# Performance work log

Measured on AMD Instinct MI355X. Metric: run time of the kernel, lower is better.

Reference implementation:

```python
import jax, jax.numpy as jnp
import numpy as np
from functools import partial


def deform_sample(inp, dy, dx):
    """Bilinear sample inp[b,c] at (y+dy[b,c,y,x], x+dx[b,c,y,x]) with zero padding.
    inp, dy, dx: [B, C, H, W] -> [B, C, H, W]. Matches torchvision deform_conv2d
    with 1x1 kernel and offset_groups == C (one offset pair per channel)."""
    B, C, H, W = inp.shape
    ys = jnp.arange(H, dtype=inp.dtype)[None, None, :, None] + dy  # [B,C,H,W]
    xs = jnp.arange(W, dtype=inp.dtype)[None, None, None, :] + dx
    y0f = jnp.floor(ys)
    x0f = jnp.floor(xs)
    wy = ys - y0f
    wx = xs - x0f
    y0 = y0f.astype(jnp.int32)
    x0 = x0f.astype(jnp.int32)
    flat = inp.reshape(B, C, H * W)

    def gather(yi, xi):
        valid = (yi >= 0) & (yi < H) & (xi >= 0) & (xi < W)
        idx = jnp.clip(yi, 0, H - 1) * W + jnp.clip(xi, 0, W - 1)
        v = jnp.take_along_axis(flat, idx.reshape(B, C, H * W), axis=2).reshape(B, C, H, W)
        return jnp.where(valid, v, jnp.zeros((), inp.dtype))

    return ((1 - wy) * (1 - wx) * gather(y0, x0)
            + (1 - wy) * wx * gather(y0, x0 + 1)
            + wy * (1 - wx) * gather(y0 + 1, x0)
            + wy * wx * gather(y0 + 1, x0 + 1))


def atm_layer(x, offset, w_weight, w_bias, h_weight, h_bias, local_weight, local_bias,
              fc1_w, fc1_b, fc2_w, fc2_b, proj_w, proj_b):
    B, H, W, C = x.shape
    x_nchw = jnp.transpose(x, (0, 3, 1, 2))  # [B,C,H,W]
    zeros = jnp.zeros_like(x_nchw)

    # ATM along w: offset[:, :C] is x-offset (offset_t[:,1::2]), y-offset 0
    sw = deform_sample(x_nchw, zeros, offset[:, :C])
    w = jnp.einsum('bchw,oc->bhwo', sw, w_weight) + w_bias  # [B,H,W,C]

    # ATM along h: offset[:, C:] is y-offset (offset_t[:,0::2]), x-offset 0
    sh = deform_sample(x_nchw, offset[:, C:], zeros)
    h = jnp.einsum('bchw,oc->bhwo', sh, h_weight) + h_bias

    # depthwise 5x5 conv, padding 2
    c = jax.lax.conv_general_dilated(
        x_nchw, local_weight, window_strides=(1, 1), padding=((2, 2), (2, 2)),
        feature_group_count=C, dimension_numbers=('NCHW', 'OIHW', 'NCHW'))
    c = jnp.transpose(c, (0, 2, 3, 1)) + local_bias  # [B,H,W,C]

    # gating MLP: global average -> fc1 -> GELU -> fc2 -> softmax over 3 branches
    a = (w + h + c).mean(axis=(1, 2))  # [B,C]
    a = jax.nn.gelu(a @ fc1_w.T + fc1_b, approximate=False)
    a = a @ fc2_w.T + fc2_b  # [B,3C]
    a = jnp.transpose(a.reshape(B, C, 3), (2, 0, 1))  # [3,B,C]
    a = jax.nn.softmax(a, axis=0)[:, :, None, None, :]  # [3,B,1,1,C]

    out = w * a[0] + h * a[1] + c * a[2]
    out = out @ proj_w.T + proj_b
    return out


def setup_inputs() -> dict:
    C = 256
    B, H, W = 16, 64, 64
    key = jax.random.key(0)
    ks = jax.random.split(key, 16)
    bnd = 1.0 / np.sqrt(C)
    hid = C // 4
    return {
        'x': jax.random.normal(ks[0], (B, H, W, C), jnp.float32),
        'offset': jax.random.normal(ks[1], (B, 2 * C, H, W), jnp.float32),
        'w_weight': jax.random.uniform(ks[2], (C, C), jnp.float32, -bnd, bnd),
        'w_bias': jax.random.uniform(ks[3], (C,), jnp.float32, -bnd, bnd),
        'h_weight': jax.random.uniform(ks[4], (C, C), jnp.float32, -bnd, bnd),
        'h_bias': jax.random.uniform(ks[5], (C,), jnp.float32, -bnd, bnd),
        'local_weight': jax.random.uniform(ks[6], (C, 1, 5, 5), jnp.float32, -0.2, 0.2),
        'local_bias': jax.random.uniform(ks[7], (C,), jnp.float32, -0.2, 0.2),
        'fc1_w': jax.random.uniform(ks[8], (hid, C), jnp.float32, -bnd, bnd),
        'fc1_b': jax.random.uniform(ks[9], (hid,), jnp.float32, -bnd, bnd),
        'fc2_w': jax.random.uniform(ks[10], (3 * C, hid), jnp.float32, -1.0 / np.sqrt(hid), 1.0 / np.sqrt(hid)),
        'fc2_b': jax.random.uniform(ks[11], (3 * C,), jnp.float32, -1.0 / np.sqrt(hid), 1.0 / np.sqrt(hid)),
        'proj_w': jax.random.uniform(ks[12], (C, C), jnp.float32, -bnd, bnd),
        'proj_b': jax.random.uniform(ks[13], (C,), jnp.float32, -bnd, bnd),
    }


def reference(x, offset, w_weight, w_bias, h_weight, h_bias, local_weight, local_bias,
              fc1_w, fc1_b, fc2_w, fc2_b, proj_w, proj_b):
    return atm_layer(x, offset, w_weight, w_bias, h_weight, h_bias, local_weight,
                     local_bias, fc1_w, fc1_b, fc2_w, fc2_b, proj_w, proj_b)
```

## Files before the change

### kernel.cpp

```cpp
#include <hip/hip_runtime.h>
#include <hip/hip_bf16.h>

typedef _Float16 half4_t __attribute__((ext_vector_type(4)));
typedef _Float16 half8 __attribute__((ext_vector_type(8)));
typedef float f32x4 __attribute__((ext_vector_type(4)));

#define BB 16
#define HH 64
#define WW2 64
#define CC 256

__global__ __launch_bounds__(256) void k_pre(
    const float* __restrict__ Ww, const float* __restrict__ Wh,
    const float* __restrict__ pw,
    _Float16* __restrict__ WwT, _Float16* __restrict__ WhT,
    _Float16* __restrict__ pf, float* __restrict__ sums)
{
  __shared__ _Float16 tile[64][65];
  const int blk = blockIdx.x;
  const int t = threadIdx.x;

  if (blk < 32) {
    const int nt = blk & 3, kt = (blk >> 2) & 3, mat = blk >> 4;
    const float* src = mat ? Wh : Ww;
    _Float16* dst = mat ? WhT : WwT;
    const int n0 = nt * 64, k0 = kt * 64;
    const int sl = t & 63;
    #pragma unroll
    for (int p = 0; p < 16; p++) {
      int chl = (t >> 6) + p * 4;
      tile[chl][sl] = (_Float16)src[(size_t)(n0 + chl) * 256 + k0 + sl];
    }
    __syncthreads();
    #pragma unroll
    for (int p = 0; p < 2; p++) {
      int pl = (t >> 3) + p * 32;
      int c8 = (t & 7) * 8;
      half8 hv;
      #pragma unroll
      for (int r = 0; r < 8; r++) hv[r] = tile[c8 + r][pl];
      *(half8*)(dst + (size_t)(k0 + pl) * 256 + n0 + c8) = hv;
    }
  } else if (blk < 80) {
    sums[(blk - 32) * 256 + t] = 0.f;
  } else {
    int i = (blk - 80) * 2048 + t * 8;
    float4 v0 = *(const float4*)(pw + i);
    float4 v1 = *(const float4*)(pw + i + 4);
    half8 h = {(_Float16)v0.x, (_Float16)v0.y, (_Float16)v0.z, (_Float16)v0.w,
               (_Float16)v1.x, (_Float16)v1.y, (_Float16)v1.z, (_Float16)v1.w};
    *(half8*)(pf + i) = h;
  }
}

__global__ __launch_bounds__(256) void k_trans(const float* __restrict__ off,
                                               _Float16* __restrict__ offAT,
                                               _Float16* __restrict__ offBT)
{
  __shared__ _Float16 tile[64][65];
  const int blk = blockIdx.x;
  const int st   = blk & 63;
  const int cht  = (blk >> 6) & 3;
  const int half = (blk >> 8) & 1;
  const int b    = blk >> 9;
  const int t = threadIdx.x;

  const int s0 = st * 64;
  const int ch0 = half * 256 + cht * 64;
  const float* src = off + ((size_t)b * 512 + ch0) * 4096 + s0;
  const int sl = t & 63;
  #pragma unroll
  for (int p = 0; p < 16; p++) {
    int chl = (t >> 6) + p * 4;
    tile[chl][sl] = (_Float16)src[(size_t)chl * 4096 + sl];
  }
  __syncthreads();

  _Float16* dst = (half == 0) ? offAT : offBT;
  #pragma unroll
  for (int p = 0; p < 2; p++) {
    int pl = (t >> 3) + p * 32;
    int c8 = (t & 7) * 8;
    half8 hv;
    #pragma unroll
    for (int r = 0; r < 8; r++) hv[r] = tile[c8 + r][pl];
    int s = s0 + pl;
    size_t pix = (half == 0) ? ((size_t)b * 4096 + s)
                             : ((size_t)b * 4096 + (s & 63) * 64 + (s >> 6));
    *(half8*)(dst + pix * 256 + cht * 64 + c8) = hv;
  }
}

__global__ __launch_bounds__(256) void k_samp(
    const float* __restrict__ x, const _Float16* __restrict__ offA,
    const float* __restrict__ lw,
    _Float16* __restrict__ swb, _Float16* __restrict__ cvb,
    float* __restrict__ ssw, float* __restrict__ scv)
{
  __shared__ _Float16 xr[WW2 * CC];

  const int work = (blockIdx.x & 7) * 128 + (blockIdx.x >> 3);
  const int b = work >> 6, y = work & 63;
  const int t = threadIdx.x;
  const int c = t;

  const float* xrow_src = x + (size_t)(b * HH + y) * WW2 * CC;
  #pragma unroll
  for (int p = 0; p < 16; p++) {
    int i = p * 1024 + t * 4;
    float4 v = *(const float4*)(xrow_src + i);
    half4_t h = {(_Float16)v.x, (_Float16)v.y, (_Float16)v.z, (_Float16)v.w};
    *(half4_t*)(xr + i) = h;
  }

  float wgt[25];
  #pragma unroll
  for (int q = 0; q < 25; q++) wgt[q] = lw[c * 25 + q];

  const float* xb = x + (size_t)b * HH * WW2 * CC + c;
  const float* rp[5];
  bool yv[5];
  #pragma unroll
  for (int ky = 0; ky < 5; ky++) {
    int yy = y + ky - 2;
    yv[ky] = (yy >= 0 && yy < HH);
    rp[ky] = xb + (size_t)(yv[ky] ? yy : 0) * WW2 * CC;
  }

  _Float16* cp = cvb + ((size_t)b * 4096 + y * 64) * CC + c;
  float acc5[5] = {0.f, 0.f, 0.f, 0.f, 0.f};
  float acv = 0.f;

  #pragma unroll 5
  for (int u = 0; u < 70; ++u) {
    acc5[(u + 2) % 5] = 0.f;
    if (u < 64) {
      float c0 = yv[0] ? rp[0][u * CC] : 0.f;
      float c1 = yv[1] ? rp[1][u * CC] : 0.f;
      float c2 = yv[2] ? rp[2][u * CC] : 0.f;
      float c3 = yv[3] ? rp[3][u * CC] : 0.f;
      float c4 = yv[4] ? rp[4][u * CC] : 0.f;
      #pragma unroll
      for (int kx = 0; kx < 5; kx++) {
        acc5[(u + 7 - kx) % 5] += wgt[0 + kx] * c0 + wgt[5 + kx] * c1 +
                                  wgt[10 + kx] * c2 + wgt[15 + kx] * c3 +
                                  wgt[20 + kx] * c4;
      }
    }
    int xi = u - 2;
    if (xi >= 0 && xi < 64) {
      float cv = acc5[(u + 3) % 5];
      cp[(size_t)xi * CC] = (_Float16)cv;
      acv += cv;
    }
  }
  atomicAdd(&scv[b * CC + c], acv);

  __syncthreads();

  const _Float16* op = offA + ((size_t)b * 4096 + y * 64) * CC + c;
  _Float16* sp = swb + ((size_t)b * 4096 + y * 64) * CC + c;
  float asw = 0.f;

  #pragma unroll 8
  for (int xi = 0; xi < 64; xi++) {
    float dx = (float)op[(size_t)xi * CC];
    float xs = (float)xi + dx;
    float xf = floorf(xs);
    float wx = xs - xf;
    int xq = (int)xf;
    float v0 = (xq >= 0 && xq < WW2) ? (float)xr[xq * CC + c] : 0.f;
    float v1 = (xq + 1 >= 0 && xq + 1 < WW2) ? (float)xr[(xq + 1) * CC + c] : 0.f;
    float swv = (1.f - wx) * v0 + wx * v1;
    sp[(size_t)xi * CC] = (_Float16)swv;
    asw += swv;
  }
  atomicAdd(&ssw[b * CC + c], asw);
}

__global__ __launch_bounds__(256) void k_col(
    const float* __restrict__ x, const _Float16* __restrict__ offBT,
    _Float16* __restrict__ shb, float* __restrict__ ssh)
{
  __shared__ _Float16 xc[HH * CC];
  const int work = (blockIdx.x & 7) * 128 + (blockIdx.x >> 3);
  const int b = work >> 6, xi = work & 63;
  const int t = threadIdx.x;
  const int c = t;

  #pragma unroll
  for (int p = 0; p < 16; p++) {
    int yy = p * 4 + (t >> 6);
    int c4 = (t & 63) * 4;
    float4 v = *(const float4*)(x + ((size_t)(b * HH + yy) * WW2 + xi) * CC + c4);
    half4_t h = {(_Float16)v.x, (_Float16)v.y, (_Float16)v.z, (_Float16)v.w};
    *(half4_t*)(xc + yy * CC + c4) = h;
  }
  __syncthreads();

  const _Float16* obt = offBT + ((size_t)(b * WW2 + xi) * HH) * CC + c;
  _Float16* hp = shb + ((size_t)(b * HH) * WW2 + xi) * CC + c;
  float ash = 0.f;
  #pragma unroll 8
  for (int yy = 0; yy < 64; yy++) {
    float dy = (float)obt[(size_t)yy * CC];
    float ys = (float)yy + dy;
    float yf = floorf(ys);
    float wy = ys - yf;
    int yq = (int)yf;
    float u0 = (yq >= 0 && yq < HH) ? (float)xc[yq * CC + c] : 0.f;
    float u1 = (yq + 1 >= 0 && yq + 1 < HH) ? (float)xc[(yq + 1) * CC + c] : 0.f;
    float shv = (1.f - wy) * u0 + wy * u1;
    hp[(size_t)yy * WW2 * CC] = (_Float16)shv;
    ash += shv;
  }
  atomicAdd(&ssh[b * CC + c], ash);
}

__global__ __launch_bounds__(256) void k_gate(
    const float* __restrict__ ssw, const float* __restrict__ ssh, const float* __restrict__ scv,
    const float* __restrict__ Ww, const float* __restrict__ bw,
    const float* __restrict__ Wh, const float* __restrict__ bh,
    const float* __restrict__ blc,
    const float* __restrict__ fc1w, const float* __restrict__ fc1b,
    const float* __restrict__ fc2w, const float* __restrict__ fc2b,
    _Float16* __restrict__ gh, float* __restrict__ bcomb)
{
  __shared__ float sswl[CC], sshl[CC], avgl[CC], tl[64];
  const int b = blockIdx.x, tid = threadIdx.x;
  sswl[tid] = ssw[b * CC + tid];
  sshl[tid] = ssh[b * CC + tid];
  __syncthreads();

  float acc = scv[b * CC + tid];
  for (int c = 0; c < CC; c++)
    acc += sswl[c] * Ww[tid * CC + c] + sshl[c] * Wh[tid * CC + c];
  avgl[tid] = acc * (1.f / (HH * WW2)) + bw[tid] + bh[tid] + blc[tid];
  __syncthreads();

  if (tid < 64) {
    float a = fc1b[tid];
    for (int o = 0; o < CC; o++) a += avgl[o] * fc1w[tid * CC + o];
    tl[tid] = 0.5f * a * (1.f + erff(a * 0.70710678118654752f));
  }
  __syncthreads();

  float g[3];
  #pragma unroll
  for (int j = 0; j < 3; j++) {
    float a = fc2b[tid * 3 + j];
    for (int k = 0; k < 64; k++) a += tl[k] * fc2w[(tid * 3 + j) * 64 + k];
    g[j] = a;
  }
  float m = fmaxf(g[0], fmaxf(g[1], g[2]));
  float e0 = expf(g[0] - m), e1 = expf(g[1] - m), e2 = expf(g[2] - m);
  float inv = 1.f / (e0 + e1 + e2);
  float a0 = e0 * inv, a1 = e1 * inv, a2 = e2 * inv;
  gh[(0 * BB + b) * CC + tid] = (_Float16)a0;
  gh[(1 * BB + b) * CC + tid] = (_Float16)a1;
  gh[(2 * BB + b) * CC + tid] = (_Float16)a2;
  bcomb[b * CC + tid] = a0 * bw[tid] + a1 * bh[tid] + a2 * blc[tid];
}

__global__ __launch_bounds__(256) void k_mats(
    const _Float16* __restrict__ pf, const _Float16* __restrict__ gh,
    const _Float16* __restrict__ WwT, const _Float16* __restrict__ WhT,
    const float* __restrict__ bcomb, const float* __restrict__ pb,
    _Float16* __restrict__ Bcat, float* __restrict__ bias_out)
{
  const int blk = (blockIdx.x & 7) * 16 + (blockIdx.x >> 3);
  const int ob = blk & 3;
  const int br = (blk >> 2) & 1;
  const int b  = blk >> 3;
  const int o0 = ob * 64;
  const int tid = threadIdx.x;
  const int wid = tid >> 6, l = tid & 63;
  const int n0 = wid * 64;
  const int lr = l & 15;
  const int kg = (l >> 4) * 8;
  const int jr = (l >> 4) * 4;

  const _Float16* WT  = br ? WhT : WwT;
  const _Float16* ghb = gh + (size_t)(br * BB + b) * CC;

  f32x4 acc[4][4];
  #pragma unroll
  for (int mi = 0; mi < 4; mi++)
    #pragma unroll
    for (int ni = 0; ni < 4; ni++) acc[mi][ni] = (f32x4){0.f, 0.f, 0.f, 0.f};

  #pragma unroll
  for (int ks = 0; ks < 8; ks++) {
    half8 gv = *(const half8*)(ghb + kg + ks * 32);
    half8 a[4], bbv[4];
    #pragma unroll
    for (int mi = 0; mi < 4; mi++)
      a[mi] = *(const half8*)(pf + (size_t)(o0 + mi * 16 + lr) * CC + kg + ks * 32) * gv;
    #pragma unroll
    for (int ni = 0; ni < 4; ni++)
      bbv[ni] = *(const half8*)(WT + (size_t)(n0 + ni * 16 + lr) * CC + kg + ks * 32);
    #pragma unroll
    for (int mi = 0; mi < 4; mi++)
      #pragma unroll
      for (int ni = 0; ni < 4; ni++)
        acc[mi][ni] = __builtin_amdgcn_mfma_f32_16x16x32_f16(a[mi], bbv[ni], acc[mi][ni], 0, 0, 0);
  }

  #pragma unroll
  for (int ni = 0; ni < 4; ni++) {
    int kcol = n0 + ni * 16 + lr;
    #pragma unroll
    for (int mi = 0; mi < 4; mi++) {
      #pragma unroll
      for (int j = 0; j < 4; j++) {
        int o = o0 + mi * 16 + jr + j;
        Bcat[((size_t)b * CC + o) * 512 + br * 256 + kcol] = (_Float16)acc[mi][ni][j];
      }
    }
  }

  if (br == 0) {
    int o_l = tid >> 2, part = tid & 3;
    const _Float16* pr = pf + (size_t)(o0 + o_l) * CC + part * 64;
    const float* bc = bcomb + b * CC + part * 64;
    float s = 0.f;
    #pragma unroll
    for (int i = 0; i < 8; i++) {
      half8 h = *(const half8*)(pr + i * 8);
      #pragma unroll
      for (int r = 0; r < 8; r++) s += (float)h[r] * bc[i * 8 + r];
    }
    s += __shfl_xor(s, 1);
    s += __shfl_xor(s, 2);
    if (part == 0) bias_out[b * CC + o0 + o_l] = s + pb[o0 + o_l];
  }
}

#define APAD 264
__global__ __launch_bounds__(256) void k_gemm(
    const _Float16* __restrict__ swb, const _Float16* __restrict__ shb,
    const _Float16* __restrict__ cvb, const _Float16* __restrict__ Bcat,
    const _Float16* __restrict__ pf, const _Float16* __restrict__ a2h,
    const float* __restrict__ bias_out, float* __restrict__ out)
{
  __shared__ _Float16 smem[64 * APAD];

  const int work = (blockIdx.x & 7) * 128 + (blockIdx.x >> 3);
  const int r0 = work * 64;
  const int b = work >> 6;
  const int tid = threadIdx.x;
  const int wid = tid >> 6, l = tid & 63;
  const int n0 = wid * 64;
  const int lr = l & 15;
  const int kg = (l >> 4) * 8;
  const int jr = (l >> 4) * 4;

  const _Float16* bq = Bcat + ((size_t)b * CC + n0 + lr) * 512 + kg;

  f32x4 acc[4][4];
  #pragma unroll
  for (int mi = 0; mi < 4; mi++)
    #pragma unroll
    for (int ni = 0; ni < 4; ni++) acc[mi][ni] = (f32x4){0.f, 0.f, 0.f, 0.f};

  half8 st[8];
  {
    const _Float16* g = swb + (size_t)r0 * CC;
    #pragma unroll
    for (int p = 0; p < 8; p++) st[p] = *(const half8*)(g + p * 2048 + tid * 8);
    #pragma unroll
    for (int p = 0; p < 8; p++) {
      int i = p * 2048 + tid * 8;
      *(half8*)(smem + (i >> 8) * APAD + (i & 255)) = st[p];
    }
  }
  __syncthreads();
  {
    const _Float16* g = shb + (size_t)r0 * CC;
    #pragma unroll
    for (int p = 0; p < 8; p++) st[p] = *(const half8*)(g + p * 2048 + tid * 8);
  }
  #pragma unroll
  for (int ks = 0; ks < 8; ks++) {
    half8 a[4], bbv[4];
    #pragma unroll
    for (int mi = 0; mi < 4; mi++)
      a[mi] = *(const half8*)(smem + (mi * 16 + lr) * APAD + kg + ks * 32);
    #pragma unroll
    for (int ni = 0; ni < 4; ni++)
      bbv[ni] = *(const half8*)(bq + (size_t)ni * 16 * 512 + ks * 32);
    #pragma unroll
    for (int mi = 0; mi < 4; mi++)
      #pragma unroll
      for (int ni = 0; ni < 4; ni++)
        acc[mi][ni] = __builtin_amdgcn_mfma_f32_16x16x32_f16(a[mi], bbv[ni], acc[mi][ni], 0, 0, 0);
  }
  __syncthreads();
  #pragma unroll
  for (int p = 0; p < 8; p++) {
    int i = p * 2048 + tid * 8;
    *(half8*)(smem + (i >> 8) * APAD + (i & 255)) = st[p];
  }
  __syncthreads();
  {
    const _Float16* g = cvb + (size_t)r0 * CC;
    #pragma unroll
    for (int p = 0; p < 8; p++) st[p] = *(const half8*)(g + p * 2048 + tid * 8);
  }
  #pragma unroll
  for (int ks = 0; ks < 8; ks++) {
    half8 a[4], bbv[4];
    #pragma unroll
    for (int mi = 0; mi < 4; mi++)
      a[mi] = *(const half8*)(smem + (mi * 16 + lr) * APAD + kg + ks * 32);
    #pragma unroll
    for (int ni = 0; ni < 4; ni++)
      bbv[ni] = *(const half8*)(bq + (size_t)ni * 16 * 512 + 256 + ks * 32);
    #pragma unroll
    for (int mi = 0; mi < 4; mi++)
      #pragma unroll
      for (int ni = 0; ni < 4; ni++)
        acc[mi][ni] = __builtin_amdgcn_mfma_f32_16x16x32_f16(a[mi], bbv[ni], acc[mi][ni], 0, 0, 0);
  }
  __syncthreads();
  #pragma unroll
  for (int p = 0; p < 8; p++) {
    int i = p * 2048 + tid * 8;
    *(half8*)(smem + (i >> 8) * APAD + (i & 255)) = st[p];
  }
  __syncthreads();
  const _Float16* a2b = a2h + (size_t)b * CC;
  #pragma unroll
  for (int ks = 0; ks < 8; ks++) {
    half8 a2v = *(const half8*)(a2b + kg + ks * 32);
    half8 a[4], bbv[4];
    #pragma unroll
    for (int mi = 0; mi < 4; mi++)
      a[mi] = *(const half8*)(smem + (mi * 16 + lr) * APAD + kg + ks * 32);
    #pragma unroll
    for (int ni = 0; ni < 4; ni++)
      bbv[ni] = *(const half8*)(pf + (size_t)(n0 + ni * 16 + lr) * CC + kg + ks * 32) * a2v;
    #pragma unroll
    for (int mi = 0; mi < 4; mi++)
      #pragma unroll
      for (int ni = 0; ni < 4; ni++)
        acc[mi][ni] = __builtin_amdgcn_mfma_f32_16x16x32_f16(a[mi], bbv[ni], acc[mi][ni], 0, 0, 0);
  }

  #pragma unroll
  for (int ni = 0; ni < 4; ni++) {
    int col = n0 + ni * 16 + lr;
    float bo = bias_out[b * CC + col];
    #pragma unroll
    for (int mi = 0; mi < 4; mi++) {
      #pragma unroll
      for (int j = 0; j < 4; j++) {
        size_t idx = (size_t)(r0 + mi * 16 + jr + j) * CC + col;
        out[idx] = acc[mi][ni][j] + bo;
      }
    }
  }
}

extern "C" void kernel_launch(void* const* d_in, const int* in_sizes, int n_in,
                              void* d_out, int out_size, void* d_ws, size_t ws_size,
                              hipStream_t stream)
{
  const float* x    = (const float*)d_in[0];
  const float* off  = (const float*)d_in[1];
  const float* Ww   = (const float*)d_in[2];
  const float* bw   = (const float*)d_in[3];
  const float* Wh   = (const float*)d_in[4];
  const float* bh   = (const float*)d_in[5];
  const float* lw   = (const float*)d_in[6];
  const float* blc  = (const float*)d_in[7];
  const float* fc1w = (const float*)d_in[8];
  const float* fc1b = (const float*)d_in[9];
  const float* fc2w = (const float*)d_in[10];
  const float* fc2b = (const float*)d_in[11];
  const float* pw   = (const float*)d_in[12];
  const float* pb   = (const float*)d_in[13];
  float* out = (float*)d_out;

  char* ws = (char*)d_ws;
  _Float16* shb   = (_Float16*)(ws + 0);
  _Float16* offAT = (_Float16*)(ws + 33554432);
  _Float16* offBT = (_Float16*)(ws + 67108864);
  _Float16* swb   = (_Float16*)(ws + 67108864);
  _Float16* Bcat  = (_Float16*)(ws + 100663296);
  _Float16* cvb   = (_Float16*)(ws + 104857600);
  _Float16* pf    = (_Float16*)(ws + 138412032);
  _Float16* gh    = (_Float16*)(ws + 138543104);
  float* bcomb    = (float*)(ws + 138567680);
  float* bias_out = (float*)(ws + 138584064);
  _Float16* WwT = (_Float16*)((char*)d_out + 0);
  _Float16* WhT = (_Float16*)((char*)d_out + 131072);
  float* sums   = (float*)((char*)d_out + 262144);
  float* ssw = sums, *ssh = sums + 4096, *scv = sums + 8192;

  k_pre<<<112, 256, 0, stream>>>(Ww, Wh, pw, WwT, WhT, pf, sums);
  k_trans<<<8192, 256, 0, stream>>>(off, offAT, offBT);
  k_col<<<BB * WW2, 256, 0, stream>>>(x, offBT, shb, ssh);
  k_samp<<<BB * HH, 256, 0, stream>>>(x, offAT, lw, swb, cvb, ssw, scv);
  k_gate<<<BB, 256, 0, stream>>>(ssw, ssh, scv, Ww, bw, Wh, bh, blc,
                                 fc1w, fc1b, fc2w, fc2b, gh, bcomb);
  k_mats<<<128, 256, 0, stream>>>(pf, gh, WwT, WhT, bcomb, pb, Bcat, bias_out);
  k_gemm<<<1024, 256, 0, stream>>>(swb, shb, cvb, Bcat, pf, gh + 2 * BB * CC,
                                   bias_out, out);
}
```

Before: 292.1 us.

## Fuse offset transpose, width sampling, conv and weight prep into one kernel

Merges k_pre, k_trans and k_samp into a single k_stage1 launch. The width-direction deformable sampling now runs directly on the transposed offset tile in shared memory, so the offAT intermediate is no longer written to or read back from global memory. The global atomics for channel sums are replaced by per-row partial sums written to workspace and reduced in k_gate, which also removes the zeroing pass. This cuts two launches and one large round trip through memory. In exchange, k_gate takes on a 64-step reduction per channel, and the workspace layout is reshuffled so that Bcat now overlaps the partial-sum buffers.

```diff
diff --git a/kernel.cpp b/kernel.cpp
--- a/kernel.cpp
+++ b/kernel.cpp
@@ -10,177 +10,171 @@
 #define WW2 64
 #define CC 256
 
-__global__ __launch_bounds__(256) void k_pre(
+__global__ __launch_bounds__(256) void k_stage1(
+    const float* __restrict__ x, const float* __restrict__ off,
+    const float* __restrict__ lw,
     const float* __restrict__ Ww, const float* __restrict__ Wh,
     const float* __restrict__ pw,
+    _Float16* __restrict__ swb, _Float16* __restrict__ offBT,
+    _Float16* __restrict__ cvb,
     _Float16* __restrict__ WwT, _Float16* __restrict__ WhT,
-    _Float16* __restrict__ pf, float* __restrict__ sums)
+    _Float16* __restrict__ pf,
+    float* __restrict__ sswp, float* __restrict__ scvp)
 {
   __shared__ _Float16 tile[64][65];
-  const int blk = blockIdx.x;
+  __shared__ _Float16 xr[64][68];
+  __shared__ float red[4][64];
+
+  const int work = (blockIdx.x & 7) * 1160 + (blockIdx.x >> 3);
   const int t = threadIdx.x;
 
-  if (blk < 32) {
-    const int nt = blk & 3, kt = (blk >> 2) & 3, mat = blk >> 4;
-    const float* src = mat ? Wh : Ww;
-    _Float16* dst = mat ? WhT : WwT;
-    const int n0 = nt * 64, k0 = kt * 64;
+  if (work < 8192) {
+    const int st   = work & 63;
+    const int cht  = (work >> 6) & 3;
+    const int half = (work >> 8) & 1;
+    const int b    = work >> 9;
+    const int ch0 = half * 256 + cht * 64;
+    const float* src = off + ((size_t)b * 512 + ch0) * 4096 + st * 64;
     const int sl = t & 63;
     #pragma unroll
     for (int p = 0; p < 16; p++) {
       int chl = (t >> 6) + p * 4;
-      tile[chl][sl] = (_Float16)src[(size_t)(n0 + chl) * 256 + k0 + sl];
-    }
-    __syncthreads();
-    #pragma unroll
-    for (int p = 0; p < 2; p++) {
-      int pl = (t >> 3) + p * 32;
-      int c8 = (t & 7) * 8;
-      half8 hv;
-      #pragma unroll
-      for (int r = 0; r < 8; r++) hv[r] = tile[c8 + r][pl];
-      *(half8*)(dst + (size_t)(k0 + pl) * 256 + n0 + c8) = hv;
-    }
-  } else if (blk < 80) {
-    sums[(blk - 32) * 256 + t] = 0.f;
+      tile[chl][sl] = (_Float16)src[(size_t)chl * 4096 + sl];
+    }
+
+    if (half == 0) {
+      const float* xs_src = x + ((size_t)(b * 64 + st) * 64) * 256 + cht * 64;
+      const int xrow = t >> 2;
+      const int c16 = (t & 3) * 16;
+      #pragma unroll
+      for (int j = 0; j < 4; j++) {
+        float4 v = *(const float4*)(xs_src + (size_t)xrow * 256 + c16 + j * 4);
+        half4_t h = {(_Float16)v.x, (_Float16)v.y, (_Float16)v.z, (_Float16)v.w};
+        *(half4_t*)(&xr[xrow][c16 + j * 4]) = h;
+      }
+      __syncthreads();
+
+      const int cl = t & 63, xg = t >> 6;
+      const int cg = cht * 64 + cl;
+      _Float16* sp = swb + ((size_t)(b * 64 + st) * 64) * 256 + cg;
+      float asw = 0.f;
+      #pragma unroll
+      for (int k = 0; k < 16; k++) {
+        int xi = xg * 16 + k;
+        float dx = (float)tile[cl][xi];
+        float xs2 = (float)xi + dx;
+        float xf = floorf(xs2);
+        float wx = xs2 - xf;
+        int xq = (int)xf;
+        float v0 = (xq >= 0 && xq < 64) ? (float)xr[xq][cl] : 0.f;
+        float v1 = (xq + 1 >= 0 && xq + 1 < 64) ? (float)xr[xq + 1][cl] : 0.f;
+        float swv = (1.f - wx) * v0 + wx * v1;
+        sp[(size_t)xi * 256] = (_Float16)swv;
+        asw += swv;
+      }
+      red[xg][cl] = asw;
+      __syncthreads();
+      if (t < 64)
+        sswp[((size_t)b * 64 + st) * 256 + cht * 64 + t] =
+            red[0][t] + red[1][t] + red[2][t] + red[3][t];
+    } else {
+      __syncthreads();
+      #pragma unroll
+      for (int p = 0; p < 2; p++) {
+        int pl = (t >> 3) + p * 32;
+        int c8 = (t & 7) * 8;
+        half8 hv;
+        #pragma unroll
+        for (int r = 0; r < 8; r++) hv[r] = tile[c8 + r][pl];
+        int s = st * 64 + pl;
+        size_t pix = (size_t)b * 4096 + (s & 63) * 64 + (s >> 6);
+        *(half8*)(offBT + pix * 256 + cht * 64 + c8) = hv;
+      }
+    }
+  } else if (work < 9216) {
+    const int w2 = work - 8192;
+    const int b = w2 >> 6, y = w2 & 63;
+    const int c = t;
+
+    float wgt[25];
+    #pragma unroll
+    for (int q = 0; q < 25; q++) wgt[q] = lw[c * 25 + q];
+
+    const float* xb = x + (size_t)b * HH * WW2 * CC + c;
+    const float* rp[5];
+    bool yv[5];
+    #pragma unroll
+    for (int ky = 0; ky < 5; ky++) {
+      int yy = y + ky - 2;
+      yv[ky] = (yy >= 0 && yy < HH);
+      rp[ky] = xb + (size_t)(yv[ky] ? yy : 0) * WW2 * CC;
+    }
+
+    _Float16* cp = cvb + ((size_t)b * 4096 + y * 64) * CC + c;
+    float acc5[5] = {0.f, 0.f, 0.f, 0.f, 0.f};
+    float acv = 0.f;
+
+    #pragma unroll 5
+    for (int u = 0; u < 70; ++u) {
+      acc5[(u + 2) % 5] = 0.f;
+      if (u < 64) {
+        float c0 = yv[0] ? rp[0][u * CC] : 0.f;
+        float c1 = yv[1] ? rp[1][u * CC] : 0.f;
+        float c2 = yv[2] ? rp[2][u * CC] : 0.f;
+        float c3 = yv[3] ? rp[3][u * CC] : 0.f;
+        float c4 = yv[4] ? rp[4][u * CC] : 0.f;
+        #pragma unroll
+        for (int kx = 0; kx < 5; kx++) {
+          acc5[(u + 7 - kx) % 5] += wgt[0 + kx] * c0 + wgt[5 + kx] * c1 +
+                                    wgt[10 + kx] * c2 + wgt[15 + kx] * c3 +
+                                    wgt[20 + kx] * c4;
+        }
+      }
+      int xi = u - 2;
+      if (xi >= 0 && xi < 64) {
+        float cv = acc5[(u + 3) % 5];
+        cp[(size_t)xi * CC] = (_Float16)cv;
+        acv += cv;
+      }
+    }
+    scvp[((size_t)b * 64 + y) * 256 + c] = acv;
   } else {
-    int i = (blk - 80) * 2048 + t * 8;
-    float4 v0 = *(const float4*)(pw + i);
-    float4 v1 = *(const float4*)(pw + i + 4);
-    half8 h = {(_Float16)v0.x, (_Float16)v0.y, (_Float16)v0.z, (_Float16)v0.w,
-               (_Float16)v1.x, (_Float16)v1.y, (_Float16)v1.z, (_Float16)v1.w};
-    *(half8*)(pf + i) = h;
-  }
-}
-
-__global__ __launch_bounds__(256) void k_trans(const float* __restrict__ off,
-                                               _Float16* __restrict__ offAT,
-                                               _Float16* __restrict__ offBT)
-{
-  __shared__ _Float16 tile[64][65];
-  const int blk = blockIdx.x;
-  const int st   = blk & 63;
-  const int cht  = (blk >> 6) & 3;
-  const int half = (blk >> 8) & 1;
-  const int b    = blk >> 9;
-  const int t = threadIdx.x;
-
-  const int s0 = st * 64;
-  const int ch0 = half * 256 + cht * 64;
-  const float* src = off + ((size_t)b * 512 + ch0) * 4096 + s0;
-  const int sl = t & 63;
-  #pragma unroll
-  for (int p = 0; p < 16; p++) {
-    int chl = (t >> 6) + p * 4;
-    tile[chl][sl] = (_Float16)src[(size_t)chl * 4096 + sl];
-  }
-  __syncthreads();
-
-  _Float16* dst = (half == 0) ? offAT : offBT;
-  #pragma unroll
-  for (int p = 0; p < 2; p++) {
-    int pl = (t >> 3) + p * 32;
-    int c8 = (t & 7) * 8;
-    half8 hv;
-    #pragma unroll
-    for (int r = 0; r < 8; r++) hv[r] = tile[c8 + r][pl];
-    int s = s0 + pl;
-    size_t pix = (half == 0) ? ((size_t)b * 4096 + s)
-                             : ((size_t)b * 4096 + (s & 63) * 64 + (s >> 6));
-    *(half8*)(dst + pix * 256 + cht * 64 + c8) = hv;
-  }
-}
-
-__global__ __launch_bounds__(256) void k_samp(
-    const float* __restrict__ x, const _Float16* __restrict__ offA,
-    const float* __restrict__ lw,
-    _Float16* __restrict__ swb, _Float16* __restrict__ cvb,
-    float* __restrict__ ssw, float* __restrict__ scv)
-{
-  __shared__ _Float16 xr[WW2 * CC];
-
-  const int work = (blockIdx.x & 7) * 128 + (blockIdx.x >> 3);
-  const int b = work >> 6, y = work & 63;
-  const int t = threadIdx.x;
-  const int c = t;
-
-  const float* xrow_src = x + (size_t)(b * HH + y) * WW2 * CC;
-  #pragma unroll
-  for (int p = 0; p < 16; p++) {
-    int i = p * 1024 + t * 4;
-    float4 v = *(const float4*)(xrow_src + i);
-    half4_t h = {(_Float16)v.x, (_Float16)v.y, (_Float16)v.z, (_Float16)v.w};
-    *(half4_t*)(xr + i) = h;
-  }
-
-  float wgt[25];
-  #pragma unroll
-  for (int q = 0; q < 25; q++) wgt[q] = lw[c * 25 + q];
-
-  const float* xb = x + (size_t)b * HH * WW2 * CC + c;
-  const float* rp[5];
-  bool yv[5];
-  #pragma unroll
-  for (int ky = 0; ky < 5; ky++) {
-    int yy = y + ky - 2;
-    yv[ky] = (yy >= 0 && yy < HH);
-    rp[ky] = xb + (size_t)(yv[ky] ? yy : 0) * WW2 * CC;
-  }
-
-  _Float16* cp = cvb + ((size_t)b * 4096 + y * 64) * CC + c;
-  float acc5[5] = {0.f, 0.f, 0.f, 0.f, 0.f};
-  float acv = 0.f;
-
-  #pragma unroll 5
-  for (int u = 0; u < 70; ++u) {
-    acc5[(u + 2) % 5] = 0.f;
-    if (u < 64) {
-      float c0 = yv[0] ? rp[0][u * CC] : 0.f;
-      float c1 = yv[1] ? rp[1][u * CC] : 0.f;
-      float c2 = yv[2] ? rp[2][u * CC] : 0.f;
-      float c3 = yv[3] ? rp[3][u * CC] : 0.f;
-      float c4 = yv[4] ? rp[4][u * CC] : 0.f;
-      #pragma unroll
-      for (int kx = 0; kx < 5; kx++) {
-        acc5[(u + 7 - kx) % 5] += wgt[0 + kx] * c0 + wgt[5 + kx] * c1 +
-                                  wgt[10 + kx] * c2 + wgt[15 + kx] * c3 +
-                                  wgt[20 + kx] * c4;
-      }
-    }
-    int xi = u - 2;
-    if (xi >= 0 && xi < 64) {
-      float cv = acc5[(u + 3) % 5];
-      cp[(size_t)xi * CC] = (_Float16)cv;
-      acv += cv;
-    }
-  }
-  atomicAdd(&scv[b * CC + c], acv);
-
-  __syncthreads();
-
-  const _Float16* op = offA + ((size_t)b * 4096 + y * 64) * CC + c;
-  _Float16* sp = swb + ((size_t)b * 4096 + y * 64) * CC + c;
-  float asw = 0.f;
-
-  #pragma unroll 8
-  for (int xi = 0; xi < 64; xi++) {
-    float dx = (float)op[(size_t)xi * CC];
-    float xs = (float)xi + dx;
-    float xf = floorf(xs);
-    float wx = xs - xf;
-    int xq = (int)xf;
-    float v0 = (xq >= 0 && xq < WW2) ? (float)xr[xq * CC + c] : 0.f;
-    float v1 = (xq + 1 >= 0 && xq + 1 < WW2) ? (float)xr[(xq + 1) * CC + c] : 0.f;
-    float swv = (1.f - wx) * v0 + wx * v1;
-    sp[(size_t)xi * CC] = (_Float16)swv;
-    asw += swv;
-  }
-  atomicAdd(&ssw[b * CC + c], asw);
+    const int w3 = work - 9216;
+    if (w3 < 32) {
+      const int nt = w3 & 3, kt = (w3 >> 2) & 3, mat = w3 >> 4;
+      const float* src = mat ? Wh : Ww;
+      _Float16* dst = mat ? WhT : WwT;
+      const int n0 = nt * 64, k0 = kt * 64;
+      const int sl = t & 63;
+      #pragma unroll
+      for (int p = 0; p < 16; p++) {
+        int chl = (t >> 6) + p * 4;
+        tile[chl][sl] = (_Float16)src[(size_t)(n0 + chl) * 256 + k0 + sl];
+      }
+      __syncthreads();
+      #pragma unroll
+      for (int p = 0; p < 2; p++) {
+        int pl = (t >> 3) + p * 32;
+        int c8 = (t & 7) * 8;
+        half8 hv;
+        #pragma unroll
+        for (int r = 0; r < 8; r++) hv[r] = tile[c8 + r][pl];
+        *(half8*)(dst + (size_t)(k0 + pl) * 256 + n0 + c8) = hv;
+      }
+    } else {
+      int i = (w3 - 32) * 2048 + t * 8;
+      float4 v0 = *(const float4*)(pw + i);
+      float4 v1 = *(const float4*)(pw + i + 4);
+      half8 h = {(_Float16)v0.x, (_Float16)v0.y, (_Float16)v0.z, (_Float16)v0.w,
+                 (_Float16)v1.x, (_Float16)v1.y, (_Float16)v1.z, (_Float16)v1.w};
+      *(half8*)(pf + i) = h;
+    }
+  }
 }
 
 __global__ __launch_bounds__(256) void k_col(
     const float* __restrict__ x, const _Float16* __restrict__ offBT,
-    _Float16* __restrict__ shb, float* __restrict__ ssh)
+    _Float16* __restrict__ shb, float* __restrict__ sshp)
 {
   __shared__ _Float16 xc[HH * CC];
   const int work = (blockIdx.x & 7) * 128 + (blockIdx.x >> 3);
@@ -214,11 +208,12 @@
     hp[(size_t)yy * WW2 * CC] = (_Float16)shv;
     ash += shv;
   }
-  atomicAdd(&ssh[b * CC + c], ash);
+  sshp[((size_t)b * 64 + xi) * 256 + c] = ash;
 }
 
 __global__ __launch_bounds__(256) void k_gate(
-    const float* __restrict__ ssw, const float* __restrict__ ssh, const float* __restrict__ scv,
+    const float* __restrict__ sswp, const float* __restrict__ sshp,
+    const float* __restrict__ scvp,
     const float* __restrict__ Ww, const float* __restrict__ bw,
     const float* __restrict__ Wh, const float* __restrict__ bh,
     const float* __restrict__ blc,
@@ -228,11 +223,18 @@
 {
   __shared__ float sswl[CC], sshl[CC], avgl[CC], tl[64];
   const int b = blockIdx.x, tid = threadIdx.x;
-  sswl[tid] = ssw[b * CC + tid];
-  sshl[tid] = ssh[b * CC + tid];
-  __syncthreads();
-
-  float acc = scv[b * CC + tid];
+
+  float s_sw = 0.f, s_sh = 0.f, s_cv = 0.f;
+  for (int q = 0; q < 64; q++) {
+    s_sw += sswp[((size_t)b * 64 + q) * 256 + tid];
+    s_sh += sshp[((size_t)b * 64 + q) * 256 + tid];
+    s_cv += scvp[((size_t)b * 64 + q) * 256 + tid];
+  }
+  sswl[tid] = s_sw;
+  sshl[tid] = s_sh;
+  __syncthreads();
+
+  float acc = s_cv;
   for (int c = 0; c < CC; c++)
     acc += sswl[c] * Ww[tid * CC + c] + sshl[c] * Wh[tid * CC + c];
   avgl[tid] = acc * (1.f / (HH * WW2)) + bw[tid] + bh[tid] + blc[tid];
@@ -484,25 +486,25 @@
 
   char* ws = (char*)d_ws;
   _Float16* shb   = (_Float16*)(ws + 0);
-  _Float16* offAT = (_Float16*)(ws + 33554432);
+  _Float16* cvb   = (_Float16*)(ws + 33554432);
   _Float16* offBT = (_Float16*)(ws + 67108864);
-  _Float16* swb   = (_Float16*)(ws + 67108864);
-  _Float16* Bcat  = (_Float16*)(ws + 100663296);
-  _Float16* cvb   = (_Float16*)(ws + 104857600);
+  _Float16* swb   = (_Float16*)(ws + 100663296);
+  _Float16* Bcat  = (_Float16*)(ws + 134217728);
+  float* sswp     = (float*)(ws + 134217728);
+  float* sshp     = (float*)(ws + 135266304);
+  float* scvp     = (float*)(ws + 136314880);
   _Float16* pf    = (_Float16*)(ws + 138412032);
   _Float16* gh    = (_Float16*)(ws + 138543104);
   float* bcomb    = (float*)(ws + 138567680);
   float* bias_out = (float*)(ws + 138584064);
   _Float16* WwT = (_Float16*)((char*)d_out + 0);
   _Float16* WhT = (_Float16*)((char*)d_out + 131072);
-  float* sums   = (float*)((char*)d_out + 262144);
-  float* ssw = sums, *ssh = sums + 4096, *scv = sums + 8192;
-
-  k_pre<<<112, 256, 0, stream>>>(Ww, Wh, pw, WwT, WhT, pf, sums);
-  k_trans<<<8192, 256, 0, stream>>>(off, offAT, offBT);
-  k_col<<<BB * WW2, 256, 0, stream>>>(x, offBT, shb, ssh);
-  k_samp<<<BB * HH, 256, 0, stream>>>(x, offAT, lw, swb, cvb, ssw, scv);
-  k_gate<<<BB, 256, 0, stream>>>(ssw, ssh, scv, Ww, bw, Wh, bh, blc,
+
+  k_stage1<<<9280, 256, 0, stream>>>(x, off, lw, Ww, Wh, pw,
+                                     swb, offBT, cvb, WwT, WhT, pf,
+                                     sswp, scvp);
+  k_col<<<BB * WW2, 256, 0, stream>>>(x, offBT, shb, sshp);
+  k_gate<<<BB, 256, 0, stream>>>(sswp, sshp, scvp, Ww, bw, Wh, bh, blc,
                                  fc1w, fc1b, fc2w, fc2b, gh, bcomb);
   k_mats<<<128, 256, 0, stream>>>(pf, gh, WwT, WhT, bcomb, pb, Bcat, bias_out);
   k_gemm<<<1024, 256, 0, stream>>>(swb, shb, cvb, Bcat, pf, gh + 2 * BB * CC,
```

Result: slower. 366.4 us (+25.4%).
